# Kernel optimization log

Hardware: AMD Instinct MI355X
Metric: run time of the kernel (lower is better)

## Reference

```python
import jax, jax.numpy as jnp
import numpy as np

N = 8192
IN_F = 256
OUT_F = 128
ALPHA = 0.2
NEG = -9000000000000000.0

def setup_inputs() -> dict:
    key = jax.random.key(0)
    k1, k2, k3, k4 = jax.random.split(key, 4)
    h = jax.random.normal(k1, (N, IN_F), dtype=jnp.float32)
    adj = jax.random.randint(k2, (N, N), 0, 2, dtype=jnp.int32)
    # xavier-uniform-like params
    limW = float(np.sqrt(6.0 / (IN_F + OUT_F)))
    W = jax.random.uniform(k3, (IN_F, OUT_F), minval=-limW, maxval=limW, dtype=jnp.float32)
    lima = float(np.sqrt(6.0 / (2 * OUT_F + 1)))
    a = jax.random.uniform(k4, (2 * OUT_F, 1), minval=-lima, maxval=lima, dtype=jnp.float32)
    return {"h": h, "adj": adj, "W": W, "a": a}

def reference(h, adj, W, a):
    Wh = h @ W  # [N, F]
    # e_ij = LeakyReLU(a1.Wh_i + a2.Wh_j) -- avoids [N,N,2F] intermediate
    a1 = a[:OUT_F, 0]  # [F]
    a2 = a[OUT_F:, 0]  # [F]
    f1 = Wh @ a1  # [N]
    f2 = Wh @ a2  # [N]
    e = jax.nn.leaky_relu(f1[:, None] + f2[None, :], negative_slope=ALPHA)  # [N,N]
    att = jnp.where(adj > 0, e, jnp.float32(NEG))
    att = jax.nn.softmax(att, axis=1)
    h_prime = att @ Wh  # [N, F]
    return h_prime
```

## Files before the change

kernel.cpp:

```cpp
#include <hip/hip_runtime.h>
#include <hip/hip_bf16.h>

#define N    8192
#define INF  256
#define OUTF 128
#define ALPHA 0.2f

typedef __attribute__((ext_vector_type(8))) short bf16x8;
typedef __attribute__((ext_vector_type(4))) float f32x4;

__device__ __forceinline__ unsigned short f2bf(float x) {
    union { float f; unsigned u; } v; v.f = x;
    unsigned r = v.u + 0x7fff + ((v.u >> 16) & 1);
    return (unsigned short)(r >> 16);
}
__device__ __forceinline__ float bf2f(unsigned short b) {
    union { unsigned u; float f; } v; v.u = ((unsigned)b) << 16;
    return v.f;
}

__global__ __launch_bounds__(256) void k1_wh(
        const float* __restrict__ h, const float* __restrict__ W,
        const float* __restrict__ a,
        unsigned short* __restrict__ WhTb, float* __restrict__ f1, float* __restrict__ f2) {
    __shared__ float hs[8][INF];
    const int t  = threadIdx.x;
    const int i0 = blockIdx.x * 8;

    #pragma unroll
    for (int u = 0; u < 2; ++u) {
        int idx = u * 256 + t;
        int r   = idx >> 6;
        int kq  = idx & 63;
        *(float4*)&hs[r][kq * 4] = *(const float4*)(h + (size_t)(i0 + r) * INF + kq * 4);
    }
    __syncthreads();

    const int rg = t >> 5;
    const int ct = t & 31;
    float acc[4] = {0.f, 0.f, 0.f, 0.f};

    #pragma unroll 8
    for (int k = 0; k < INF; ++k) {
        float4 wv = *(const float4*)(W + (size_t)k * OUTF + ct * 4);
        float  hx = hs[rg][k];
        acc[0] += hx * wv.x; acc[1] += hx * wv.y;
        acc[2] += hx * wv.z; acc[3] += hx * wv.w;
    }

    const int r0 = i0 + rg;
    const int jb = r0 >> 5;
    const int jo = r0 & 31;
    #pragma unroll
    for (int cc = 0; cc < 4; ++cc)
        WhTb[(size_t)jb * 4096 + (ct * 4 + cc) * 32 + jo] = f2bf(acc[cc]);

    const float4 a1v = *(const float4*)(a + ct * 4);
    const float4 a2v = *(const float4*)(a + OUTF + ct * 4);
    float p1 = acc[0]*a1v.x + acc[1]*a1v.y + acc[2]*a1v.z + acc[3]*a1v.w;
    float p2 = acc[0]*a2v.x + acc[1]*a2v.y + acc[2]*a2v.z + acc[3]*a2v.w;
    #pragma unroll
    for (int off = 16; off > 0; off >>= 1) {
        p1 += __shfl_down(p1, off, 32);
        p2 += __shfl_down(p2, off, 32);
    }
    if (ct == 0) { f1[r0] = p1; f2[r0] = p2; }
}

struct PFA { int4 a0, a1; };

__device__ __forceinline__ PFA ldadj(const int* __restrict__ ap, int jt) {
    PFA p;
    p.a0 = *(const int4*)(ap + (size_t)jt * 32);
    p.a1 = *(const int4*)(ap + (size_t)jt * 32 + 4);
    return p;
}

#define EXP1(AV, FV, IDX)                                                   \
    {                                                                       \
        float s_ = f1r + (FV);                                              \
        float e_ = s_ > 0.f ? s_ : ALPHA * s_;                              \
        float p_ = ((AV) > 0) ? __expf(e_) : 0.f;                           \
        unsigned short pb_ = f2bf(p_);                                      \
        afrag[IDX] = (short)pb_;                                            \
        dsum += bf2f(pb_);                                                  \
    }

#define K2STEP(PFV, JT)                                                     \
    {                                                                       \
        const unsigned short* wp_ = WhTb + ((size_t)(w * 64 + (JT))) * 4096 + laneb; \
        bf16x8 b0_ = *(const bf16x8*)(wp_);                                 \
        bf16x8 b1_ = *(const bf16x8*)(wp_ + 512);                           \
        bf16x8 b2_ = *(const bf16x8*)(wp_ + 1024);                          \
        bf16x8 b3_ = *(const bf16x8*)(wp_ + 1536);                          \
        bf16x8 b4_ = *(const bf16x8*)(wp_ + 2048);                          \
        bf16x8 b5_ = *(const bf16x8*)(wp_ + 2560);                          \
        bf16x8 b6_ = *(const bf16x8*)(wp_ + 3072);                          \
        bf16x8 b7_ = *(const bf16x8*)(wp_ + 3584);                          \
        float4 F0_ = *(const float4*)(f2p + (size_t)(JT) * 32);             \
        float4 F1_ = *(const float4*)(f2p + (size_t)(JT) * 32 + 4);         \
        int4 A0_ = PFV.a0, A1_ = PFV.a1;                                    \
        if ((JT) + 2 < NT) PFV = ldadj(adjp, (JT) + 2);                     \
        bf16x8 afrag;                                                       \
        EXP1(A0_.x, F0_.x, 0) EXP1(A0_.y, F0_.y, 1)                         \
        EXP1(A0_.z, F0_.z, 2) EXP1(A0_.w, F0_.w, 3)                         \
        EXP1(A1_.x, F1_.x, 4) EXP1(A1_.y, F1_.y, 5)                         \
        EXP1(A1_.z, F1_.z, 6) EXP1(A1_.w, F1_.w, 7)                         \
        acc0 = __builtin_amdgcn_mfma_f32_16x16x32_bf16(afrag, b0_, acc0, 0, 0, 0); \
        acc1 = __builtin_amdgcn_mfma_f32_16x16x32_bf16(afrag, b1_, acc1, 0, 0, 0); \
        acc2 = __builtin_amdgcn_mfma_f32_16x16x32_bf16(afrag, b2_, acc2, 0, 0, 0); \
        acc3 = __builtin_amdgcn_mfma_f32_16x16x32_bf16(afrag, b3_, acc3, 0, 0, 0); \
        acc4 = __builtin_amdgcn_mfma_f32_16x16x32_bf16(afrag, b4_, acc4, 0, 0, 0); \
        acc5 = __builtin_amdgcn_mfma_f32_16x16x32_bf16(afrag, b5_, acc5, 0, 0, 0); \
        acc6 = __builtin_amdgcn_mfma_f32_16x16x32_bf16(afrag, b6_, acc6, 0, 0, 0); \
        acc7 = __builtin_amdgcn_mfma_f32_16x16x32_bf16(afrag, b7_, acc7, 0, 0, 0); \
    }

__global__ __launch_bounds__(256, 3) void k2_attn(
        const int* __restrict__ adj, const unsigned short* __restrict__ WhTb,
        const float* __restrict__ f1, const float* __restrict__ f2,
        float* __restrict__ out) {
    __shared__ float red[4][16][132];
    __shared__ float den_s[4][16];

    const int t    = threadIdx.x;
    const int w    = t >> 6;
    const int ln   = t & 63;
    const int m16  = ln & 15;
    const int quad = ln >> 4;
    const int i0   = blockIdx.x * 16;
    const int row  = i0 + m16;

    const float f1r = f1[row];
    const int   j0w = w * (N / 4);
    const int   NT  = (N / 4) / 32;

    const int*   adjp  = adj + (size_t)row * N + j0w + quad * 8;
    const float* f2p   = f2 + j0w + quad * 8;
    const int    laneb = m16 * 32 + quad * 8;

    f32x4 acc0 = {0.f,0.f,0.f,0.f}, acc1 = {0.f,0.f,0.f,0.f};
    f32x4 acc2 = {0.f,0.f,0.f,0.f}, acc3 = {0.f,0.f,0.f,0.f};
    f32x4 acc4 = {0.f,0.f,0.f,0.f}, acc5 = {0.f,0.f,0.f,0.f};
    f32x4 acc6 = {0.f,0.f,0.f,0.f}, acc7 = {0.f,0.f,0.f,0.f};
    float dsum = 0.f;

    PFA pf0 = ldadj(adjp, 0);
    PFA pf1 = ldadj(adjp, 1);

    for (int jt = 0; jt < NT; jt += 2) {
        K2STEP(pf0, jt)
        K2STEP(pf1, jt + 1)
    }

    dsum += __shfl_xor(dsum, 16);
    dsum += __shfl_xor(dsum, 32);
    if (quad == 0) den_s[w][m16] = dsum;

    #pragma unroll
    for (int r = 0; r < 4; ++r) {
        red[w][quad * 4 + r][0 * 16 + m16] = acc0[r];
        red[w][quad * 4 + r][1 * 16 + m16] = acc1[r];
        red[w][quad * 4 + r][2 * 16 + m16] = acc2[r];
        red[w][quad * 4 + r][3 * 16 + m16] = acc3[r];
        red[w][quad * 4 + r][4 * 16 + m16] = acc4[r];
        red[w][quad * 4 + r][5 * 16 + m16] = acc5[r];
        red[w][quad * 4 + r][6 * 16 + m16] = acc6[r];
        red[w][quad * 4 + r][7 * 16 + m16] = acc7[r];
    }
    __syncthreads();

    #pragma unroll
    for (int e = 0; e < 2; ++e) {
        int idx = e * 256 + t;
        int r   = idx >> 5;
        int c4  = (idx & 31) * 4;
        float4 s0 = *(const float4*)&red[0][r][c4];
        float4 s1 = *(const float4*)&red[1][r][c4];
        float4 s2 = *(const float4*)&red[2][r][c4];
        float4 s3 = *(const float4*)&red[3][r][c4];
        float dtot = den_s[0][r] + den_s[1][r] + den_s[2][r] + den_s[3][r];
        float inv  = 1.0f / dtot;
        float4 o;
        o.x = (s0.x + s1.x + s2.x + s3.x) * inv;
        o.y = (s0.y + s1.y + s2.y + s3.y) * inv;
        o.z = (s0.z + s1.z + s2.z + s3.z) * inv;
        o.w = (s0.w + s1.w + s2.w + s3.w) * inv;
        *(float4*)(out + (size_t)(i0 + r) * OUTF + c4) = o;
    }
}

extern "C" void kernel_launch(void* const* d_in, const int* in_sizes, int n_in,
                              void* d_out, int out_size, void* d_ws, size_t ws_size,
                              hipStream_t stream) {
    const float* h   = (const float*)d_in[0];
    const int*   adj = (const int*)  d_in[1];
    const float* W   = (const float*)d_in[2];
    const float* a   = (const float*)d_in[3];
    float* out = (float*)d_out;

    unsigned short* WhTb = (unsigned short*)d_ws;
    float* f1 = (float*)(WhTb + (size_t)N * OUTF);
    float* f2 = f1 + N;

    k1_wh  <<<N / 8, 256, 0, stream>>>(h, W, a, WhTb, f1, f2);
    k2_attn<<<N / 16, 256, 0, stream>>>(adj, WhTb, f1, f2, out);
}
```

Before: 452.3 us.

## Deepen software prefetch pipeline for adj, f2 and Wh tiles in attention kernel

Restructures the k2 main loop into a 4-step unrolled software pipeline: adjacency rows are prefetched four tiles ahead, f2 two tiles ahead, and the bf16 Wh fragments one tile ahead in double-buffered registers. This hides global-load latency behind the exp and MFMA work. It also packs probabilities with the bf16x2 conversion intrinsic and sums the denominator in fp32 rather than from the rounded bf16 values. Occupancy is lowered from 3 to 2 blocks per CU to make room for the extra registers. The risks are fewer resident waves and a small numerical mismatch between the softmax numerator and denominator.

```diff
diff --git a/kernel.cpp b/kernel.cpp
--- a/kernel.cpp
+++ b/kernel.cpp
@@ -5,6 +5,7 @@
 #define INF  256
 #define OUTF 128
 #define ALPHA 0.2f
+#define MIN2(x, y) ((x) < (y) ? (x) : (y))
 
 typedef __attribute__((ext_vector_type(8))) short bf16x8;
 typedef __attribute__((ext_vector_type(4))) float f32x4;
@@ -13,10 +14,6 @@
     union { float f; unsigned u; } v; v.f = x;
     unsigned r = v.u + 0x7fff + ((v.u >> 16) & 1);
     return (unsigned short)(r >> 16);
-}
-__device__ __forceinline__ float bf2f(unsigned short b) {
-    union { unsigned u; float f; } v; v.u = ((unsigned)b) << 16;
-    return v.f;
 }
 
 __global__ __launch_bounds__(256) void k1_wh(
@@ -68,6 +65,8 @@
 }
 
 struct PFA { int4 a0, a1; };
+struct FG  { float4 g0, g1; };
+struct BFr { bf16x8 b0, b1, b2, b3, b4, b5, b6, b7; };
 
 __device__ __forceinline__ PFA ldadj(const int* __restrict__ ap, int jt) {
     PFA p;
@@ -75,48 +74,65 @@
     p.a1 = *(const int4*)(ap + (size_t)jt * 32 + 4);
     return p;
 }
-
-#define EXP1(AV, FV, IDX)                                                   \
+__device__ __forceinline__ FG ldf2(const float* __restrict__ gp, int jt) {
+    FG g;
+    g.g0 = *(const float4*)(gp + (size_t)jt * 32);
+    g.g1 = *(const float4*)(gp + (size_t)jt * 32 + 4);
+    return g;
+}
+__device__ __forceinline__ BFr ldb(const unsigned short* __restrict__ base) {
+    BFr r;
+    r.b0 = *(const bf16x8*)(base);
+    r.b1 = *(const bf16x8*)(base + 512);
+    r.b2 = *(const bf16x8*)(base + 1024);
+    r.b3 = *(const bf16x8*)(base + 1536);
+    r.b4 = *(const bf16x8*)(base + 2048);
+    r.b5 = *(const bf16x8*)(base + 2560);
+    r.b6 = *(const bf16x8*)(base + 3072);
+    r.b7 = *(const bf16x8*)(base + 3584);
+    return r;
+}
+
+__device__ __forceinline__ float pleak(float f1r, float fv, int av, float& dsum) {
+    float s = f1r + fv;
+    float e = fmaxf(s, ALPHA * s);
+    float p = (av > 0) ? __expf(e) : 0.f;
+    dsum += p;
+    return p;
+}
+
+#define K2S(AB, GB, WB, WNEXT, JT)                                          \
     {                                                                       \
-        float s_ = f1r + (FV);                                              \
-        float e_ = s_ > 0.f ? s_ : ALPHA * s_;                              \
-        float p_ = ((AV) > 0) ? __expf(e_) : 0.f;                           \
-        unsigned short pb_ = f2bf(p_);                                      \
-        afrag[IDX] = (short)pb_;                                            \
-        dsum += bf2f(pb_);                                                  \
-    }
-
-#define K2STEP(PFV, JT)                                                     \
-    {                                                                       \
-        const unsigned short* wp_ = WhTb + ((size_t)(w * 64 + (JT))) * 4096 + laneb; \
-        bf16x8 b0_ = *(const bf16x8*)(wp_);                                 \
-        bf16x8 b1_ = *(const bf16x8*)(wp_ + 512);                           \
-        bf16x8 b2_ = *(const bf16x8*)(wp_ + 1024);                          \
-        bf16x8 b3_ = *(const bf16x8*)(wp_ + 1536);                          \
-        bf16x8 b4_ = *(const bf16x8*)(wp_ + 2048);                          \
-        bf16x8 b5_ = *(const bf16x8*)(wp_ + 2560);                          \
-        bf16x8 b6_ = *(const bf16x8*)(wp_ + 3072);                          \
-        bf16x8 b7_ = *(const bf16x8*)(wp_ + 3584);                          \
-        float4 F0_ = *(const float4*)(f2p + (size_t)(JT) * 32);             \
-        float4 F1_ = *(const float4*)(f2p + (size_t)(JT) * 32 + 4);         \
-        int4 A0_ = PFV.a0, A1_ = PFV.a1;                                    \
-        if ((JT) + 2 < NT) PFV = ldadj(adjp, (JT) + 2);                     \
-        bf16x8 afrag;                                                       \
-        EXP1(A0_.x, F0_.x, 0) EXP1(A0_.y, F0_.y, 1)                         \
-        EXP1(A0_.z, F0_.z, 2) EXP1(A0_.w, F0_.w, 3)                         \
-        EXP1(A1_.x, F1_.x, 4) EXP1(A1_.y, F1_.y, 5)                         \
-        EXP1(A1_.z, F1_.z, 6) EXP1(A1_.w, F1_.w, 7)                         \
-        acc0 = __builtin_amdgcn_mfma_f32_16x16x32_bf16(afrag, b0_, acc0, 0, 0, 0); \
-        acc1 = __builtin_amdgcn_mfma_f32_16x16x32_bf16(afrag, b1_, acc1, 0, 0, 0); \
-        acc2 = __builtin_amdgcn_mfma_f32_16x16x32_bf16(afrag, b2_, acc2, 0, 0, 0); \
-        acc3 = __builtin_amdgcn_mfma_f32_16x16x32_bf16(afrag, b3_, acc3, 0, 0, 0); \
-        acc4 = __builtin_amdgcn_mfma_f32_16x16x32_bf16(afrag, b4_, acc4, 0, 0, 0); \
-        acc5 = __builtin_amdgcn_mfma_f32_16x16x32_bf16(afrag, b5_, acc5, 0, 0, 0); \
-        acc6 = __builtin_amdgcn_mfma_f32_16x16x32_bf16(afrag, b6_, acc6, 0, 0, 0); \
-        acc7 = __builtin_amdgcn_mfma_f32_16x16x32_bf16(afrag, b7_, acc7, 0, 0, 0); \
-    }
-
-__global__ __launch_bounds__(256, 3) void k2_attn(
+        int4   A0_ = AB.a0, A1_ = AB.a1;                                    \
+        float4 F0_ = GB.g0, F1_ = GB.g1;                                    \
+        WNEXT = ldb(wb + (size_t)MIN2((JT) + 1, NT - 1) * 4096);            \
+        GB    = ldf2(f2p, MIN2((JT) + 2, NT - 1));                          \
+        AB    = ldadj(adjp, MIN2((JT) + 4, NT - 1));                        \
+        float p0_ = pleak(f1r, F0_.x, A0_.x, dsum);                         \
+        float p1_ = pleak(f1r, F0_.y, A0_.y, dsum);                         \
+        float p2_ = pleak(f1r, F0_.z, A0_.z, dsum);                         \
+        float p3_ = pleak(f1r, F0_.w, A0_.w, dsum);                         \
+        float p4_ = pleak(f1r, F1_.x, A1_.x, dsum);                         \
+        float p5_ = pleak(f1r, F1_.y, A1_.y, dsum);                         \
+        float p6_ = pleak(f1r, F1_.z, A1_.z, dsum);                         \
+        float p7_ = pleak(f1r, F1_.w, A1_.w, dsum);                         \
+        union { __hip_bfloat162 h[4]; bf16x8 v; } pk_;                      \
+        pk_.h[0] = __float22bfloat162_rn(make_float2(p0_, p1_));            \
+        pk_.h[1] = __float22bfloat162_rn(make_float2(p2_, p3_));            \
+        pk_.h[2] = __float22bfloat162_rn(make_float2(p4_, p5_));            \
+        pk_.h[3] = __float22bfloat162_rn(make_float2(p6_, p7_));            \
+        bf16x8 afrag = pk_.v;                                               \
+        acc0 = __builtin_amdgcn_mfma_f32_16x16x32_bf16(afrag, WB.b0, acc0, 0, 0, 0); \
+        acc1 = __builtin_amdgcn_mfma_f32_16x16x32_bf16(afrag, WB.b1, acc1, 0, 0, 0); \
+        acc2 = __builtin_amdgcn_mfma_f32_16x16x32_bf16(afrag, WB.b2, acc2, 0, 0, 0); \
+        acc3 = __builtin_amdgcn_mfma_f32_16x16x32_bf16(afrag, WB.b3, acc3, 0, 0, 0); \
+        acc4 = __builtin_amdgcn_mfma_f32_16x16x32_bf16(afrag, WB.b4, acc4, 0, 0, 0); \
+        acc5 = __builtin_amdgcn_mfma_f32_16x16x32_bf16(afrag, WB.b5, acc5, 0, 0, 0); \
+        acc6 = __builtin_amdgcn_mfma_f32_16x16x32_bf16(afrag, WB.b6, acc6, 0, 0, 0); \
+        acc7 = __builtin_amdgcn_mfma_f32_16x16x32_bf16(afrag, WB.b7, acc7, 0, 0, 0); \
+    }
+
+__global__ __launch_bounds__(256, 2) void k2_attn(
         const int* __restrict__ adj, const unsigned short* __restrict__ WhTb,
         const float* __restrict__ f1, const float* __restrict__ f2,
         float* __restrict__ out) {
@@ -135,9 +151,9 @@
     const int   j0w = w * (N / 4);
     const int   NT  = (N / 4) / 32;
 
-    const int*   adjp  = adj + (size_t)row * N + j0w + quad * 8;
-    const float* f2p   = f2 + j0w + quad * 8;
-    const int    laneb = m16 * 32 + quad * 8;
+    const int*            adjp = adj + (size_t)row * N + j0w + quad * 8;
+    const float*          f2p  = f2 + j0w + quad * 8;
+    const unsigned short* wb   = WhTb + (size_t)w * 64 * 4096 + (m16 * 32 + quad * 8);
 
     f32x4 acc0 = {0.f,0.f,0.f,0.f}, acc1 = {0.f,0.f,0.f,0.f};
     f32x4 acc2 = {0.f,0.f,0.f,0.f}, acc3 = {0.f,0.f,0.f,0.f};
@@ -145,12 +161,16 @@
     f32x4 acc6 = {0.f,0.f,0.f,0.f}, acc7 = {0.f,0.f,0.f,0.f};
     float dsum = 0.f;
 
-    PFA pf0 = ldadj(adjp, 0);
-    PFA pf1 = ldadj(adjp, 1);
-
-    for (int jt = 0; jt < NT; jt += 2) {
-        K2STEP(pf0, jt)
-        K2STEP(pf1, jt + 1)
+    PFA pa0 = ldadj(adjp, 0), pa1 = ldadj(adjp, 1);
+    PFA pa2 = ldadj(adjp, 2), pa3 = ldadj(adjp, 3);
+    FG  pg0 = ldf2(f2p, 0),  pg1 = ldf2(f2p, 1);
+    BFr pw0 = ldb(wb), pw1;
+
+    for (int jt = 0; jt < NT; jt += 4) {
+        K2S(pa0, pg0, pw0, pw1, jt)
+        K2S(pa1, pg1, pw1, pw0, jt + 1)
+        K2S(pa2, pg0, pw0, pw1, jt + 2)
+        K2S(pa3, pg1, pw1, pw0, jt + 3)
     }
 
     dsum += __shfl_xor(dsum, 16);
```

Measured after the change: 484.5 us. +7.1%, slower.

## Split attention columns across grid blocks with separate combine kernel

Applied to the files above, without the earlier changes.

The attention kernel now gives each wave its own 16 rows and splits the column range into 8 slices across a second grid dimension, writing partial numerators and denominators to workspace. A new combine kernel sums the partials and normalizes, replacing the in-block LDS reduction. The bf16 packing now uses paired conversion intrinsics, the denominator is summed from unrounded floats, and the occupancy hint rises to 4 blocks. This trades extra global traffic (about 32MB of partial sums) and a third launch for more independent blocks and better reuse of WhTb within a block.

```diff
diff --git a/kernel.cpp b/kernel.cpp
--- a/kernel.cpp
+++ b/kernel.cpp
@@ -5,6 +5,7 @@
 #define INF  256
 #define OUTF 128
 #define ALPHA 0.2f
+#define JS   8
 
 typedef __attribute__((ext_vector_type(8))) short bf16x8;
 typedef __attribute__((ext_vector_type(4))) float f32x4;
@@ -13,10 +14,6 @@
     union { float f; unsigned u; } v; v.f = x;
     unsigned r = v.u + 0x7fff + ((v.u >> 16) & 1);
     return (unsigned short)(r >> 16);
-}
-__device__ __forceinline__ float bf2f(unsigned short b) {
-    union { unsigned u; float f; } v; v.u = ((unsigned)b) << 16;
-    return v.f;
 }
 
 __global__ __launch_bounds__(256) void k1_wh(
@@ -76,19 +73,17 @@
     return p;
 }
 
-#define EXP1(AV, FV, IDX)                                                   \
-    {                                                                       \
-        float s_ = f1r + (FV);                                              \
-        float e_ = s_ > 0.f ? s_ : ALPHA * s_;                              \
-        float p_ = ((AV) > 0) ? __expf(e_) : 0.f;                           \
-        unsigned short pb_ = f2bf(p_);                                      \
-        afrag[IDX] = (short)pb_;                                            \
-        dsum += bf2f(pb_);                                                  \
-    }
+__device__ __forceinline__ float pleak(float f1r, float fv, int av, float& dsum) {
+    float s = f1r + fv;
+    float e = fmaxf(s, ALPHA * s);
+    float p = (av > 0) ? __expf(e) : 0.f;
+    dsum += p;
+    return p;
+}
 
 #define K2STEP(PFV, JT)                                                     \
     {                                                                       \
-        const unsigned short* wp_ = WhTb + ((size_t)(w * 64 + (JT))) * 4096 + laneb; \
+        const unsigned short* wp_ = WhTb + ((size_t)(tile0 + (JT))) * 4096 + laneb; \
         bf16x8 b0_ = *(const bf16x8*)(wp_);                                 \
         bf16x8 b1_ = *(const bf16x8*)(wp_ + 512);                           \
         bf16x8 b2_ = *(const bf16x8*)(wp_ + 1024);                          \
@@ -101,11 +96,20 @@
         float4 F1_ = *(const float4*)(f2p + (size_t)(JT) * 32 + 4);         \
         int4 A0_ = PFV.a0, A1_ = PFV.a1;                                    \
         if ((JT) + 2 < NT) PFV = ldadj(adjp, (JT) + 2);                     \
-        bf16x8 afrag;                                                       \
-        EXP1(A0_.x, F0_.x, 0) EXP1(A0_.y, F0_.y, 1)                         \
-        EXP1(A0_.z, F0_.z, 2) EXP1(A0_.w, F0_.w, 3)                         \
-        EXP1(A1_.x, F1_.x, 4) EXP1(A1_.y, F1_.y, 5)                         \
-        EXP1(A1_.z, F1_.z, 6) EXP1(A1_.w, F1_.w, 7)                         \
+        float p0_ = pleak(f1r, F0_.x, A0_.x, dsum);                         \
+        float p1_ = pleak(f1r, F0_.y, A0_.y, dsum);                         \
+        float p2_ = pleak(f1r, F0_.z, A0_.z, dsum);                         \
+        float p3_ = pleak(f1r, F0_.w, A0_.w, dsum);                         \
+        float p4_ = pleak(f1r, F1_.x, A1_.x, dsum);                         \
+        float p5_ = pleak(f1r, F1_.y, A1_.y, dsum);                         \
+        float p6_ = pleak(f1r, F1_.z, A1_.z, dsum);                         \
+        float p7_ = pleak(f1r, F1_.w, A1_.w, dsum);                         \
+        union { __hip_bfloat162 hh[4]; bf16x8 v; } pk_;                     \
+        pk_.hh[0] = __float22bfloat162_rn(make_float2(p0_, p1_));           \
+        pk_.hh[1] = __float22bfloat162_rn(make_float2(p2_, p3_));           \
+        pk_.hh[2] = __float22bfloat162_rn(make_float2(p4_, p5_));           \
+        pk_.hh[3] = __float22bfloat162_rn(make_float2(p6_, p7_));           \
+        bf16x8 afrag = pk_.v;                                               \
         acc0 = __builtin_amdgcn_mfma_f32_16x16x32_bf16(afrag, b0_, acc0, 0, 0, 0); \
         acc1 = __builtin_amdgcn_mfma_f32_16x16x32_bf16(afrag, b1_, acc1, 0, 0, 0); \
         acc2 = __builtin_amdgcn_mfma_f32_16x16x32_bf16(afrag, b2_, acc2, 0, 0, 0); \
@@ -116,27 +120,26 @@
         acc7 = __builtin_amdgcn_mfma_f32_16x16x32_bf16(afrag, b7_, acc7, 0, 0, 0); \
     }
 
-__global__ __launch_bounds__(256, 3) void k2_attn(
+__global__ __launch_bounds__(256, 4) void k2_attn(
         const int* __restrict__ adj, const unsigned short* __restrict__ WhTb,
         const float* __restrict__ f1, const float* __restrict__ f2,
-        float* __restrict__ out) {
-    __shared__ float red[4][16][132];
-    __shared__ float den_s[4][16];
-
+        float* __restrict__ num, float* __restrict__ den) {
     const int t    = threadIdx.x;
-    const int w    = t >> 6;
+    const int wv   = t >> 6;
     const int ln   = t & 63;
     const int m16  = ln & 15;
     const int quad = ln >> 4;
-    const int i0   = blockIdx.x * 16;
-    const int row  = i0 + m16;
-
-    const float f1r = f1[row];
-    const int   j0w = w * (N / 4);
-    const int   NT  = (N / 4) / 32;
-
-    const int*   adjp  = adj + (size_t)row * N + j0w + quad * 8;
-    const float* f2p   = f2 + j0w + quad * 8;
+    const int i0   = blockIdx.x * 64;
+    const int s    = blockIdx.y;
+    const int row  = i0 + wv * 16 + m16;
+
+    const float f1r  = f1[row];
+    const int   j0   = s * (N / JS);
+    const int   NT   = (N / JS) / 32;
+    const int   tile0 = s * NT;
+
+    const int*   adjp  = adj + (size_t)row * N + j0 + quad * 8;
+    const float* f2p   = f2 + j0 + quad * 8;
     const int    laneb = m16 * 32 + quad * 8;
 
     f32x4 acc0 = {0.f,0.f,0.f,0.f}, acc1 = {0.f,0.f,0.f,0.f};
@@ -155,39 +158,40 @@
 
     dsum += __shfl_xor(dsum, 16);
     dsum += __shfl_xor(dsum, 32);
-    if (quad == 0) den_s[w][m16] = dsum;
-
+    if (quad == 0) den[(size_t)s * N + row] = dsum;
+
+    float* np = num + (size_t)s * N * OUTF;
     #pragma unroll
     for (int r = 0; r < 4; ++r) {
-        red[w][quad * 4 + r][0 * 16 + m16] = acc0[r];
-        red[w][quad * 4 + r][1 * 16 + m16] = acc1[r];
-        red[w][quad * 4 + r][2 * 16 + m16] = acc2[r];
-        red[w][quad * 4 + r][3 * 16 + m16] = acc3[r];
-        red[w][quad * 4 + r][4 * 16 + m16] = acc4[r];
-        red[w][quad * 4 + r][5 * 16 + m16] = acc5[r];
-        red[w][quad * 4 + r][6 * 16 + m16] = acc6[r];
-        red[w][quad * 4 + r][7 * 16 + m16] = acc7[r];
-    }
-    __syncthreads();
-
-    #pragma unroll
-    for (int e = 0; e < 2; ++e) {
-        int idx = e * 256 + t;
-        int r   = idx >> 5;
-        int c4  = (idx & 31) * 4;
-        float4 s0 = *(const float4*)&red[0][r][c4];
-        float4 s1 = *(const float4*)&red[1][r][c4];
-        float4 s2 = *(const float4*)&red[2][r][c4];
-        float4 s3 = *(const float4*)&red[3][r][c4];
-        float dtot = den_s[0][r] + den_s[1][r] + den_s[2][r] + den_s[3][r];
-        float inv  = 1.0f / dtot;
-        float4 o;
-        o.x = (s0.x + s1.x + s2.x + s3.x) * inv;
-        o.y = (s0.y + s1.y + s2.y + s3.y) * inv;
-        o.z = (s0.z + s1.z + s2.z + s3.z) * inv;
-        o.w = (s0.w + s1.w + s2.w + s3.w) * inv;
-        *(float4*)(out + (size_t)(i0 + r) * OUTF + c4) = o;
-    }
+        const size_t orow = (size_t)(i0 + wv * 16 + quad * 4 + r) * OUTF;
+        np[orow + 0 * 16 + m16] = acc0[r];
+        np[orow + 1 * 16 + m16] = acc1[r];
+        np[orow + 2 * 16 + m16] = acc2[r];
+        np[orow + 3 * 16 + m16] = acc3[r];
+        np[orow + 4 * 16 + m16] = acc4[r];
+        np[orow + 5 * 16 + m16] = acc5[r];
+        np[orow + 6 * 16 + m16] = acc6[r];
+        np[orow + 7 * 16 + m16] = acc7[r];
+    }
+}
+
+__global__ __launch_bounds__(256) void k3_combine(
+        const float* __restrict__ num, const float* __restrict__ den,
+        float* __restrict__ out) {
+    const int idx = blockIdx.x * 256 + threadIdx.x;
+    const int row = idx >> 5;
+    const int c4  = (idx & 31) * 4;
+    float4 ns = {0.f,0.f,0.f,0.f};
+    float  ds = 0.f;
+    #pragma unroll
+    for (int s = 0; s < JS; ++s) {
+        float4 nv = *(const float4*)(num + ((size_t)s * N + row) * OUTF + c4);
+        ns.x += nv.x; ns.y += nv.y; ns.z += nv.z; ns.w += nv.w;
+        ds += den[(size_t)s * N + row];
+    }
+    const float inv = 1.0f / ds;
+    float4 o = {ns.x * inv, ns.y * inv, ns.z * inv, ns.w * inv};
+    *(float4*)(out + (size_t)row * OUTF + c4) = o;
 }
 
 extern "C" void kernel_launch(void* const* d_in, const int* in_sizes, int n_in,
@@ -200,9 +204,12 @@
     float* out = (float*)d_out;
 
     unsigned short* WhTb = (unsigned short*)d_ws;
-    float* f1 = (float*)(WhTb + (size_t)N * OUTF);
-    float* f2 = f1 + N;
-
-    k1_wh  <<<N / 8, 256, 0, stream>>>(h, W, a, WhTb, f1, f2);
-    k2_attn<<<N / 16, 256, 0, stream>>>(adj, WhTb, f1, f2, out);
-}
+    float* f1  = (float*)(WhTb + (size_t)N * OUTF);
+    float* f2  = f1 + N;
+    float* den = f2 + N;
+    float* num = den + (size_t)JS * N;
+
+    k1_wh     <<<N / 8, 256, 0, stream>>>(h, W, a, WhTb, f1, f2);
+    k2_attn   <<<dim3(N / 64, JS), 256, 0, stream>>>(adj, WhTb, f1, f2, num, den);
+    k3_combine<<<(N * OUTF / 4) / 256, 256, 0, stream>>>(num, den, out);
+}
```

Measured after the change: 473.8 us. 1.05x slower.
